# Optimization experiments

Hardware: AMD Instinct MI355X
Metric: run time of the kernel (lower is better)

Reference implementation:

```python
import jax, jax.numpy as jnp
import numpy as np

B, T, H, DH = 4, 2048, 16, 128
D = H * DH            # inner_dim = 2048
F = 4096              # mlp_inner_dim
E = 8                 # num_expert_mlp
TOP_K = 2


def setup_inputs() -> dict:
    key = jax.random.key(0)
    ks = jax.random.split(key, 5)
    s_in = 1.0 / np.sqrt(D)
    s_f = 1.0 / np.sqrt(F)
    return {
        "stm": jax.random.normal(ks[0], (B, T, H, DH), dtype=jnp.float32),
        "gate_w": jax.random.normal(ks[1], (E, D), dtype=jnp.float32) * s_in,
        "w1": jax.random.normal(ks[2], (E, F, D), dtype=jnp.float32) * s_in,
        "w2": jax.random.normal(ks[3], (E, D, F), dtype=jnp.float32) * s_f,
        "w3": jax.random.normal(ks[4], (E, F, D), dtype=jnp.float32) * s_in,
    }


def reference(stm, gate_w, w1, w2, w3):
    b, t, h, dh = stm.shape
    d = h * dh
    x = stm.reshape(b * t, d)                                   # [N, D]
    logits = x @ gate_w.T                                       # [N, E]
    top_logit, top_idx = jax.lax.top_k(logits, TOP_K)           # [N, 2]
    gw = jax.nn.softmax(top_logit.astype(jnp.float32), axis=1).astype(x.dtype)
    out = jnp.zeros_like(x)
    n_expert = w1.shape[0]
    for e in range(n_expert):
        # combine weight for expert e per token (0 if not routed)
        we = jnp.sum(jnp.where(top_idx == e, gw, jnp.zeros_like(gw)), axis=1)  # [N]
        gate = jax.nn.silu(x @ w1[e].T)                          # [N, F]
        up = x @ w3[e].T                                         # [N, F]
        y = (gate * up) @ w2[e].T                                # [N, D]
        out = out + we[:, None] * y
    return out.reshape(b, t, h, dh)
```

## Files before the change

kernel.cpp:

```cpp
#include <hip/hip_runtime.h>
#include <hip/hip_bf16.h>
#include <stdint.h>

#define N_TOK 8192
#define DIM   2048
#define FDIM  4096
#define NEXP  8

#define XB_OFF   0ull
#define HB_OFF   33554432ull
#define WB1_OFF  176160768ull
#define WB3_OFF  243269632ull
#define META_OFF 310378496ull
#define CNT_OFF   (META_OFF)
#define EBASE_OFF (META_OFF + 64ull)
#define ELIST_OFF (META_OFF + 128ull)
#define EWTS_OFF  (ELIST_OFF + 262144ull)

typedef float f32x4 __attribute__((ext_vector_type(4)));
typedef short s16x8 __attribute__((ext_vector_type(8)));

__device__ __forceinline__ uint32_t pkbf(float a, float b) {
  uint32_t ua = __builtin_bit_cast(uint32_t, a) + 0x8000u;
  uint32_t ub = __builtin_bit_cast(uint32_t, b) + 0x8000u;
  return (ua >> 16) | (ub & 0xffff0000u);
}

__device__ __forceinline__ void gld16(const void* g, void* l) {
  __builtin_amdgcn_global_load_lds(
      (__attribute__((address_space(1))) void*)g,
      (__attribute__((address_space(3))) void*)l, 16, 0, 0);
}

__global__ void zero_out_k(float* out) {
  const size_t i = ((size_t)blockIdx.x * 256 + threadIdx.x) * 4;
  *(float4*)(out + i) = make_float4(0.f, 0.f, 0.f, 0.f);
}

__global__ void init_k(int* cnt) {
  if (threadIdx.x < NEXP) cnt[threadIdx.x] = 0;
}

__global__ void router_k(const float* __restrict__ x, const float* __restrict__ gw,
                         __hip_bfloat16* __restrict__ xb, int* __restrict__ cnt,
                         int* __restrict__ elist, float* __restrict__ ewts) {
  const int n = blockIdx.x;
  const int t = threadIdx.x;
  const float* xr = x + (size_t)n * DIM;
  const float4 v0 = *(const float4*)(xr + t * 8);
  const float4 v1 = *(const float4*)(xr + t * 8 + 4);
  uint4 u;
  u.x = pkbf(v0.x, v0.y); u.y = pkbf(v0.z, v0.w);
  u.z = pkbf(v1.x, v1.y); u.w = pkbf(v1.z, v1.w);
  *(uint4*)(xb + (size_t)n * DIM + t * 8) = u;

  float p[NEXP];
#pragma unroll
  for (int e = 0; e < NEXP; ++e) {
    const float* g = gw + e * DIM + t * 8;
    const float4 g0 = *(const float4*)g;
    const float4 g1 = *(const float4*)(g + 4);
    p[e] = v0.x * g0.x + v0.y * g0.y + v0.z * g0.z + v0.w * g0.w +
           v1.x * g1.x + v1.y * g1.y + v1.z * g1.z + v1.w * g1.w;
  }
#pragma unroll
  for (int off = 32; off >= 1; off >>= 1)
#pragma unroll
    for (int e = 0; e < NEXP; ++e) p[e] += __shfl_xor(p[e], off, 64);

  __shared__ float red[4][NEXP];
  const int lane = t & 63, wv = t >> 6;
  if (lane == 0) {
#pragma unroll
    for (int e = 0; e < NEXP; ++e) red[wv][e] = p[e];
  }
  __syncthreads();
  if (t == 0) {
    float l0 = -1e30f, l1 = -1e30f;
    int e0 = 0, e1 = 0;
#pragma unroll
    for (int e = 0; e < NEXP; ++e) {
      float v = red[0][e] + red[1][e] + red[2][e] + red[3][e];
      if (v > l0) { l1 = l0; e1 = e0; l0 = v; e0 = e; }
      else if (v > l1) { l1 = v; e1 = e; }
    }
    const float ed = expf(l1 - l0);
    const float inv = 1.f / (1.f + ed);
    int s0 = atomicAdd(cnt + e0, 1);
    elist[e0 * N_TOK + s0] = n;
    ewts[e0 * N_TOK + s0] = inv;
    int s1 = atomicAdd(cnt + e1, 1);
    elist[e1 * N_TOK + s1] = (int)((uint32_t)n | 0x80000000u);
    ewts[e1 * N_TOK + s1] = ed * inv;
  }
}

__global__ void scan_k(const int* __restrict__ cnt, int* __restrict__ ebase) {
  if (threadIdx.x == 0 && blockIdx.x == 0) {
    int b = 0;
    for (int e = 0; e < NEXP; ++e) { ebase[e] = b; b += (cnt[e] + 127) & ~127; }
  }
}

__global__ void convW_k(const float* __restrict__ src, __hip_bfloat16* __restrict__ dst,
                        int r0, int nrh, int rtot, int kd) {
  const int cpr = kd / 8;
  const int total = NEXP * nrh * cpr;
  for (int i = blockIdx.x * blockDim.x + threadIdx.x; i < total;
       i += gridDim.x * blockDim.x) {
    const int e = i / (nrh * cpr);
    const int rem = i - e * nrh * cpr;
    const int lr = rem / cpr;
    const int c = rem - lr * cpr;
    const float* s = src + ((size_t)e * rtot + r0 + lr) * (size_t)kd + c * 8;
    const float4 a = *(const float4*)s;
    const float4 b = *(const float4*)(s + 4);
    uint4 u;
    u.x = pkbf(a.x, a.y); u.y = pkbf(a.z, a.w);
    u.z = pkbf(b.x, b.y); u.w = pkbf(b.z, b.w);
    *(uint4*)(dst + ((size_t)e * nrh + lr) * (size_t)kd + c * 8) = u;
  }
}

__global__ __launch_bounds__(256, 2) void moe_up_k(
    const __hip_bfloat16* __restrict__ xb, const __hip_bfloat16* __restrict__ w1b,
    const __hip_bfloat16* __restrict__ w3b, __hip_bfloat16* __restrict__ hb,
    const int* __restrict__ cnt, const int* __restrict__ ebase,
    const int* __restrict__ elist, int noff) {
  const int e = blockIdx.z;
  const int count = cnt[e];
  const int mt = blockIdx.y;
  if (mt * 128 >= count) return;
  const int bn0 = blockIdx.x * 128;
  const int ncol0 = noff + bn0;

  __shared__ char lds[49152];
  const int t = threadIdx.x;
  const int lane = t & 63, wv = t >> 6;
  const int wr = wv >> 1, wc = wv & 1;
  const int* lst = elist + e * N_TOK;
  const size_t hrow0 = (size_t)ebase[e] + (size_t)mt * 128;

  const int r0 = t >> 2;
  const int ks = (t & 3) ^ ((r0 >> 1) & 3);
  size_t sA[2], sB1[2];
  int ldsO[2];
#pragma unroll
  for (int i = 0; i < 2; ++i) {
    const int r = r0 + i * 64;
    int idx = mt * 128 + r;
    if (idx >= count) idx = 0;
    const size_t tok = (size_t)(lst[idx] & 0x7fffffff);
    sA[i] = tok * DIM + ks * 8;
    sB1[i] = ((size_t)e * 2048 + bn0 + r) * DIM + ks * 8;
    ldsO[i] = i * 4096 + wv * 1024;
  }

  const int fr = lane & 15;
  const int swzc = ((lane >> 4) ^ ((fr >> 1) & 3)) << 4;
  const int aoff = (wr * 64 + fr) * 64 + swzc;
  const int boff = (wc * 64 + fr) * 64 + swzc;

  f32x4 accG[4][4], accU[4][4];
#pragma unroll
  for (int mi = 0; mi < 4; ++mi)
#pragma unroll
    for (int ni = 0; ni < 4; ++ni) {
      accG[mi][ni] = {0.f, 0.f, 0.f, 0.f};
      accU[mi][ni] = {0.f, 0.f, 0.f, 0.f};
    }

  auto stage = [&](int k0, int b) {
#pragma unroll
    for (int i = 0; i < 2; ++i)
      gld16(xb + sA[i] + k0, lds + b * 8192 + ldsO[i]);
#pragma unroll
    for (int i = 0; i < 2; ++i)
      gld16(w1b + sB1[i] + k0, lds + 16384 + b * 8192 + ldsO[i]);
#pragma unroll
    for (int i = 0; i < 2; ++i)
      gld16(w3b + sB1[i] + k0, lds + 32768 + b * 8192 + ldsO[i]);
  };

  stage(0, 0);
  __syncthreads();

  int b = 0;
  for (int kt = 0; kt < DIM / 32; ++kt) {
    const int nk = (kt + 1) * 32;
    if (nk < DIM) stage(nk, b ^ 1);
    s16x8 af[4], b1f[4], b3f[4];
#pragma unroll
    for (int mi = 0; mi < 4; ++mi)
      af[mi] = *(const s16x8*)(lds + b * 8192 + aoff + mi * 1024);
#pragma unroll
    for (int ni = 0; ni < 4; ++ni) {
      b1f[ni] = *(const s16x8*)(lds + 16384 + b * 8192 + boff + ni * 1024);
      b3f[ni] = *(const s16x8*)(lds + 32768 + b * 8192 + boff + ni * 1024);
    }
#pragma unroll
    for (int mi = 0; mi < 4; ++mi)
#pragma unroll
      for (int ni = 0; ni < 4; ++ni) {
        accG[mi][ni] = __builtin_amdgcn_mfma_f32_16x16x32_bf16(
            af[mi], b1f[ni], accG[mi][ni], 0, 0, 0);
        accU[mi][ni] = __builtin_amdgcn_mfma_f32_16x16x32_bf16(
            af[mi], b3f[ni], accU[mi][ni], 0, 0, 0);
      }
    __syncthreads();
    b ^= 1;
  }

  const int erow = (lane >> 4) * 4;
  const int ecol = lane & 15;
#pragma unroll
  for (int mi = 0; mi < 4; ++mi)
#pragma unroll
    for (int ni = 0; ni < 4; ++ni) {
      const size_t cb = ncol0 + wc * 64 + ni * 16 + ecol;
#pragma unroll
      for (int j = 0; j < 4; ++j) {
        const size_t r = hrow0 + wr * 64 + mi * 16 + erow + j;
        const float g = accG[mi][ni][j];
        const float uu = accU[mi][ni][j];
        const float h = g / (1.f + __expf(-g)) * uu;
        hb[r * FDIM + cb] = __float2bfloat16(h);
      }
    }
}

__global__ __launch_bounds__(256, 2) void moe_down_k(
    const __hip_bfloat16* __restrict__ hb, const __hip_bfloat16* __restrict__ w2b,
    float* __restrict__ out, const int* __restrict__ cnt,
    const int* __restrict__ ebase, const int* __restrict__ elist,
    const float* __restrict__ ewts) {
  const int e = blockIdx.z;
  const int count = cnt[e];
  const int mt = blockIdx.y;
  if (mt * 128 >= count) return;
  const int bn0 = blockIdx.x * 256;

  __shared__ char lds[49152];
  const int t = threadIdx.x;
  const int lane = t & 63, wv = t >> 6;
  const int wr = wv >> 1, wc = wv & 1;
  const int* lst = elist + e * N_TOK;
  const size_t hrow0 = (size_t)ebase[e] + (size_t)mt * 128;

  const int r0 = t >> 2;
  const int ks = (t & 3) ^ ((r0 >> 1) & 3);
  size_t sA[2], sB[2];
  int ldsO[2];
#pragma unroll
  for (int i = 0; i < 2; ++i) {
    const int r = r0 + i * 64;
    sA[i] = (hrow0 + r) * (size_t)FDIM + ks * 8;
    sB[i] = ((size_t)e * 2048 + bn0 + r) * (size_t)FDIM + ks * 8;
    ldsO[i] = i * 4096 + wv * 1024;
  }
  const size_t sBp = 128 * (size_t)FDIM;

  const int fr = lane & 15;
  const int swzc = ((lane >> 4) ^ ((fr >> 1) & 3)) << 4;
  const int aoff = (wr * 64 + fr) * 64 + swzc;
  const int boff = (wc * 64 + fr) * 64 + swzc;

  f32x4 accP[2][4][4];
#pragma unroll
  for (int p = 0; p < 2; ++p)
#pragma unroll
    for (int mi = 0; mi < 4; ++mi)
#pragma unroll
      for (int ni = 0; ni < 4; ++ni) accP[p][mi][ni] = {0.f, 0.f, 0.f, 0.f};

  auto stage = [&](int k0, int b) {
#pragma unroll
    for (int i = 0; i < 2; ++i)
      gld16(hb + sA[i] + k0, lds + b * 8192 + ldsO[i]);
#pragma unroll
    for (int i = 0; i < 2; ++i)
      gld16(w2b + sB[i] + k0, lds + 16384 + b * 8192 + ldsO[i]);
#pragma unroll
    for (int i = 0; i < 2; ++i)
      gld16(w2b + sB[i] + sBp + k0, lds + 32768 + b * 8192 + ldsO[i]);
  };

  stage(0, 0);
  __syncthreads();

  int b = 0;
  for (int kt = 0; kt < FDIM / 32; ++kt) {
    const int nk = (kt + 1) * 32;
    if (nk < FDIM) stage(nk, b ^ 1);
    s16x8 af[4], b0f[4], b1f[4];
#pragma unroll
    for (int mi = 0; mi < 4; ++mi)
      af[mi] = *(const s16x8*)(lds + b * 8192 + aoff + mi * 1024);
#pragma unroll
    for (int ni = 0; ni < 4; ++ni) {
      b0f[ni] = *(const s16x8*)(lds + 16384 + b * 8192 + boff + ni * 1024);
      b1f[ni] = *(const s16x8*)(lds + 32768 + b * 8192 + boff + ni * 1024);
    }
#pragma unroll
    for (int mi = 0; mi < 4; ++mi)
#pragma unroll
      for (int ni = 0; ni < 4; ++ni) {
        accP[0][mi][ni] = __builtin_amdgcn_mfma_f32_16x16x32_bf16(
            af[mi], b0f[ni], accP[0][mi][ni], 0, 0, 0);
        accP[1][mi][ni] = __builtin_amdgcn_mfma_f32_16x16x32_bf16(
            af[mi], b1f[ni], accP[1][mi][ni], 0, 0, 0);
      }
    __syncthreads();
    b ^= 1;
  }

  const int erow = (lane >> 4) * 4;
  const int ecol = lane & 15;
#pragma unroll
  for (int mi = 0; mi < 4; ++mi)
#pragma unroll
    for (int j = 0; j < 4; ++j) {
      const int i = mt * 128 + wr * 64 + mi * 16 + erow + j;
      if (i < count) {
        const uint32_t info = (uint32_t)lst[i];
        const int tok = (int)(info & 0x7fffffffu);
        const float wt = ewts[e * N_TOK + i];
        float* prow = out + (size_t)tok * DIM;
#pragma unroll
        for (int p = 0; p < 2; ++p)
#pragma unroll
          for (int ni = 0; ni < 4; ++ni) {
            const int cb = bn0 + p * 128 + wc * 64 + ni * 16 + ecol;
            atomicAdd(prow + cb, wt * accP[p][mi][ni][j]);
          }
      }
    }
}

extern "C" void kernel_launch(void* const* d_in, const int* in_sizes, int n_in,
                              void* d_out, int out_size, void* d_ws, size_t ws_size,
                              hipStream_t stream) {
  const float* stm = (const float*)d_in[0];
  const float* gw = (const float*)d_in[1];
  const float* w1 = (const float*)d_in[2];
  const float* w2 = (const float*)d_in[3];
  const float* w3 = (const float*)d_in[4];
  float* out = (float*)d_out;
  char* ws = (char*)d_ws;

  __hip_bfloat16* xb = (__hip_bfloat16*)(ws + XB_OFF);
  __hip_bfloat16* hb = (__hip_bfloat16*)(ws + HB_OFF);
  __hip_bfloat16* wb1 = (__hip_bfloat16*)(ws + WB1_OFF);
  __hip_bfloat16* wb3 = (__hip_bfloat16*)(ws + WB3_OFF);
  __hip_bfloat16* w2full = (__hip_bfloat16*)(ws + WB1_OFF);
  int* cnt = (int*)(ws + CNT_OFF);
  int* ebase = (int*)(ws + EBASE_OFF);
  int* elist = (int*)(ws + ELIST_OFF);
  float* ewts = (float*)(ws + EWTS_OFF);

  init_k<<<1, 64, 0, stream>>>(cnt);
  router_k<<<N_TOK, 256, 0, stream>>>(stm, gw, xb, cnt, elist, ewts);
  scan_k<<<1, 64, 0, stream>>>(cnt, ebase);
  zero_out_k<<<N_TOK * DIM / 1024, 256, 0, stream>>>(out);

  const dim3 gUp(16, 64, 8);
  const dim3 gDn(8, 64, 8);

  convW_k<<<2048, 256, 0, stream>>>(w1, wb1, 0, 2048, FDIM, DIM);
  convW_k<<<2048, 256, 0, stream>>>(w3, wb3, 0, 2048, FDIM, DIM);
  moe_up_k<<<gUp, 256, 0, stream>>>(xb, wb1, wb3, hb, cnt, ebase, elist, 0);
  convW_k<<<2048, 256, 0, stream>>>(w1, wb1, 2048, 2048, FDIM, DIM);
  convW_k<<<2048, 256, 0, stream>>>(w3, wb3, 2048, 2048, FDIM, DIM);
  moe_up_k<<<gUp, 256, 0, stream>>>(xb, wb1, wb3, hb, cnt, ebase, elist, 2048);

  convW_k<<<4096, 256, 0, stream>>>(w2, w2full, 0, 2048, DIM, FDIM);
  moe_down_k<<<gDn, 256, 0, stream>>>(hb, w2full, out, cnt, ebase, elist, ewts);
}
```

Before: 1.428 ms.

## Triple-buffer down-projection LDS pipeline with vmcnt-based waits and expert-major grid

```diff
diff --git a/kernel.cpp b/kernel.cpp
--- a/kernel.cpp
+++ b/kernel.cpp
@@ -234,13 +234,14 @@
     float* __restrict__ out, const int* __restrict__ cnt,
     const int* __restrict__ ebase, const int* __restrict__ elist,
     const float* __restrict__ ewts) {
-  const int e = blockIdx.z;
+  constexpr int NT = FDIM / 32;
+  const int e = blockIdx.x;
   const int count = cnt[e];
   const int mt = blockIdx.y;
   if (mt * 128 >= count) return;
-  const int bn0 = blockIdx.x * 256;
-
-  __shared__ char lds[49152];
+  const int bn0 = blockIdx.z * 256;
+
+  __shared__ char lds[73728];
   const int t = threadIdx.x;
   const int lane = t & 63, wv = t >> 6;
   const int wr = wv >> 1, wc = wv & 1;
@@ -273,33 +274,41 @@
 #pragma unroll
       for (int ni = 0; ni < 4; ++ni) accP[p][mi][ni] = {0.f, 0.f, 0.f, 0.f};
 
-  auto stage = [&](int k0, int b) {
-#pragma unroll
-    for (int i = 0; i < 2; ++i)
-      gld16(hb + sA[i] + k0, lds + b * 8192 + ldsO[i]);
-#pragma unroll
-    for (int i = 0; i < 2; ++i)
-      gld16(w2b + sB[i] + k0, lds + 16384 + b * 8192 + ldsO[i]);
-#pragma unroll
-    for (int i = 0; i < 2; ++i)
-      gld16(w2b + sB[i] + sBp + k0, lds + 32768 + b * 8192 + ldsO[i]);
+  auto stage = [&](int kt, int b) {
+    const int k0 = kt * 32;
+    char* base = lds + b * 24576;
+#pragma unroll
+    for (int i = 0; i < 2; ++i)
+      gld16(hb + sA[i] + k0, base + ldsO[i]);
+#pragma unroll
+    for (int i = 0; i < 2; ++i)
+      gld16(w2b + sB[i] + k0, base + 8192 + ldsO[i]);
+#pragma unroll
+    for (int i = 0; i < 2; ++i)
+      gld16(w2b + sB[i] + sBp + k0, base + 16384 + ldsO[i]);
   };
 
   stage(0, 0);
-  __syncthreads();
-
-  int b = 0;
-  for (int kt = 0; kt < FDIM / 32; ++kt) {
-    const int nk = (kt + 1) * 32;
-    if (nk < FDIM) stage(nk, b ^ 1);
+  stage(1, 1);
+  asm volatile("s_waitcnt vmcnt(6)" ::: "memory");
+  __builtin_amdgcn_sched_barrier(0);
+  __builtin_amdgcn_s_barrier();
+  __builtin_amdgcn_sched_barrier(0);
+
+  int bR = 0, bS = 2;
+#pragma unroll 3
+  for (int kt = 0; kt < NT; ++kt) {
+    const int t2 = (kt + 2 < NT) ? kt + 2 : NT - 1;
+    stage(t2, bS);
+    char* base = lds + bR * 24576;
     s16x8 af[4], b0f[4], b1f[4];
 #pragma unroll
     for (int mi = 0; mi < 4; ++mi)
-      af[mi] = *(const s16x8*)(lds + b * 8192 + aoff + mi * 1024);
+      af[mi] = *(const s16x8*)(base + aoff + mi * 1024);
 #pragma unroll
     for (int ni = 0; ni < 4; ++ni) {
-      b0f[ni] = *(const s16x8*)(lds + 16384 + b * 8192 + boff + ni * 1024);
-      b1f[ni] = *(const s16x8*)(lds + 32768 + b * 8192 + boff + ni * 1024);
+      b0f[ni] = *(const s16x8*)(base + 8192 + boff + ni * 1024);
+      b1f[ni] = *(const s16x8*)(base + 16384 + boff + ni * 1024);
     }
 #pragma unroll
     for (int mi = 0; mi < 4; ++mi)
@@ -310,8 +319,12 @@
         accP[1][mi][ni] = __builtin_amdgcn_mfma_f32_16x16x32_bf16(
             af[mi], b1f[ni], accP[1][mi][ni], 0, 0, 0);
       }
-    __syncthreads();
-    b ^= 1;
+    asm volatile("s_waitcnt vmcnt(6)" ::: "memory");
+    __builtin_amdgcn_sched_barrier(0);
+    __builtin_amdgcn_s_barrier();
+    __builtin_amdgcn_sched_barrier(0);
+    bR = (bR == 2) ? 0 : bR + 1;
+    bS = (bS == 2) ? 0 : bS + 1;
   }
 
   const int erow = (lane >> 4) * 4;
```

Measured after the change: 1.384 ms. 1.03x faster.
